# Kernel optimization log

Hardware: AMD Instinct MI355X
Metric: run time of the kernel (lower is better)

Reference implementation:

```python
import jax, jax.numpy as jnp
import numpy as np

N_NODES = 50000
N_EDGES = 800000
IN_CH = 64
HID = 128
OUT_AGE, OUT_SEX, OUT_ETH = 21, 2, 5


def _glorot(key, shape):
    fan_in, fan_out = shape
    lim = float(np.sqrt(6.0 / (fan_in + fan_out)))
    return jax.random.uniform(key, shape, jnp.float32, -lim, lim)


def sage_conv(x, src, dst, Wl, Wr, b, n_nodes):
    # PyG SAGEConv (mean aggr): out = lin_l(mean_{j->i} x_j) + lin_r(x_i) + bias
    msg_sum = jax.ops.segment_sum(x[src], dst, num_segments=n_nodes)  # [N, d]
    deg = jax.ops.segment_sum(jnp.ones((src.shape[0],), x.dtype), dst,
                              num_segments=n_nodes)  # [N]
    mean = msg_sum / jnp.maximum(deg, 1.0)[:, None]
    return mean @ Wl + x @ Wr + b


def setup_inputs() -> dict:
    key = jax.random.key(0)
    ks = jax.random.split(key, 16)
    x = jax.random.normal(ks[0], (N_NODES, IN_CH), jnp.float32)
    edge_src = jax.random.randint(ks[1], (N_EDGES,), 0, N_NODES)
    edge_dst = jax.random.randint(ks[2], (N_EDGES,), 0, N_NODES)
    dims = [(IN_CH, HID), (HID, HID), (HID, HID),
            (HID, OUT_AGE), (HID, OUT_SEX), (HID, OUT_ETH)]
    names = ['1', '2', '3', 'age', 'sex', 'eth']
    inp = {'x': x, 'edge_src': edge_src, 'edge_dst': edge_dst}
    for i, (nm, (di, do)) in enumerate(zip(names, dims)):
        inp[f'Wl_{nm}'] = _glorot(ks[3 + 2 * i], (di, do))
        inp[f'Wr_{nm}'] = _glorot(ks[4 + 2 * i], (di, do))
        inp[f'b_{nm}'] = jnp.zeros((do,), jnp.float32)
    return inp


def reference(x, edge_src, edge_dst,
              Wl_1, Wr_1, b_1, Wl_2, Wr_2, b_2, Wl_3, Wr_3, b_3,
              Wl_age, Wr_age, b_age, Wl_sex, Wr_sex, b_sex,
              Wl_eth, Wr_eth, b_eth):
    n = x.shape[0]
    h = jax.nn.relu(sage_conv(x, edge_src, edge_dst, Wl_1, Wr_1, b_1, n))
    h = jax.nn.relu(sage_conv(h, edge_src, edge_dst, Wl_2, Wr_2, b_2, n))
    h = jax.nn.relu(sage_conv(h, edge_src, edge_dst, Wl_3, Wr_3, b_3, n))
    age = sage_conv(h, edge_src, edge_dst, Wl_age, Wr_age, b_age, n)
    sex = sage_conv(h, edge_src, edge_dst, Wl_sex, Wr_sex, b_sex, n)
    eth = sage_conv(h, edge_src, edge_dst, Wl_eth, Wr_eth, b_eth, n)
    return (age, sex, eth)
```

## Files before the change

kernel.cpp:

```cpp
#include <hip/hip_runtime.h>
#include <hip/hip_bf16.h>


typedef __attribute__((ext_vector_type(8))) short bf16x8;
typedef __attribute__((ext_vector_type(4))) float f32x4;

#define NBSH 7
#define EPW  4096

__device__ __forceinline__ unsigned short f2b(float f) {
    __hip_bfloat16 h = __float2bfloat16(f);
    return *reinterpret_cast<unsigned short*>(&h);
}
__device__ __forceinline__ float b2f(unsigned short u) {
    __hip_bfloat16 h;
    *reinterpret_cast<unsigned short*>(&h) = u;
    return __bfloat162float(h);
}

__global__ void bucket_hist(const int* __restrict__ dst, int* __restrict__ ghist,
                            int n_edges, int nb) {
    __shared__ int lh[512];
    int tid = threadIdx.x;
    for (int i = tid; i < 512; i += 256) lh[i] = 0;
    __syncthreads();
    int stride = gridDim.x * blockDim.x;
    for (int e = blockIdx.x * blockDim.x + tid; e < n_edges; e += stride)
        atomicAdd(&lh[dst[e] >> NBSH], 1);
    __syncthreads();
    for (int i = tid; i < nb; i += 256)
        if (lh[i]) atomicAdd(&ghist[i], lh[i]);
}

__global__ void scan_buckets(const int* __restrict__ hist, int* __restrict__ base,
                             int* __restrict__ cur, int nb, int n_edges) {
    __shared__ int tmp[512];
    int t = threadIdx.x;
    int v = (t < nb) ? hist[t] : 0;
    tmp[t] = v;
    __syncthreads();
    for (int off = 1; off < 512; off <<= 1) {
        int u = (t >= off) ? tmp[t - off] : 0;
        __syncthreads();
        tmp[t] += u;
        __syncthreads();
    }
    if (t < nb) {
        base[t] = tmp[t] - v;
        cur[t] = tmp[t] - v;
    }
    if (t == 0) base[nb] = n_edges;
}

__global__ __launch_bounds__(512) void bin_edges_lds(
    const int* __restrict__ src, const int* __restrict__ dst,
    int* __restrict__ bkt_cur, uint2* __restrict__ ebuf, int n_edges, int nb) {
    __shared__ int hist[512];
    __shared__ int hbase[513];
    __shared__ int hcur[512];
    __shared__ uint2 sorted[EPW];
    int tid = threadIdx.x;
    int chunk0 = blockIdx.x * EPW;
    int cnt = min(EPW, n_edges - chunk0);
    hist[tid] = 0;
    __syncthreads();
    for (int i = tid; i < cnt; i += 512) atomicAdd(&hist[dst[chunk0 + i] >> NBSH], 1);
    __syncthreads();
    int v = hist[tid];
    hbase[tid] = v;
    __syncthreads();
    for (int off = 1; off < 512; off <<= 1) {
        int u = (tid >= off) ? hbase[tid - off] : 0;
        __syncthreads();
        hbase[tid] += u;
        __syncthreads();
    }
    int excl = hbase[tid] - v;
    __syncthreads();
    hbase[tid] = excl;
    hcur[tid] = excl;
    if (tid == 511) hbase[512] = excl + v;
    __syncthreads();
    for (int i = tid; i < cnt; i += 512) {
        int s = src[chunk0 + i];
        int d = dst[chunk0 + i];
        int p = atomicAdd(&hcur[d >> NBSH], 1);
        sorted[p] = make_uint2((unsigned)s, (unsigned)d);
    }
    __syncthreads();
    int cntb = hbase[tid + 1] - hbase[tid];
    int gb = 0;
    if (tid < nb && cntb > 0) gb = atomicAdd(&bkt_cur[tid], cntb);
    hist[tid] = gb;
    __syncthreads();
    for (int i = tid; i < cnt; i += 512) {
        uint2 ed = sorted[i];
        int b = (int)(ed.y >> NBSH);
        ebuf[hist[b] + (i - hbase[b])] = ed;
    }
}

__global__ void sort_bucket(const uint2* __restrict__ ebuf, const int* __restrict__ bkt_base,
                            int* __restrict__ row_start, int* __restrict__ col,
                            int n_nodes, int n_edges) {
    __shared__ int hist[128];
    __shared__ int sc[128];
    __shared__ int hcur[128];
    int b = blockIdx.x, tid = threadIdx.x;
    int lo = b << NBSH;
    if (tid < 128) hist[tid] = 0;
    __syncthreads();
    int s = bkt_base[b], t = bkt_base[b + 1];
    for (int i = s + tid; i < t; i += 256) atomicAdd(&hist[(int)ebuf[i].y - lo], 1);
    __syncthreads();
    if (tid < 128) sc[tid] = hist[tid];
    __syncthreads();
    for (int off = 1; off < 128; off <<= 1) {
        int u = (tid < 128 && tid >= off) ? sc[tid - off] : 0;
        __syncthreads();
        if (tid < 128) sc[tid] += u;
        __syncthreads();
    }
    if (tid < 128) {
        int excl = sc[tid] - hist[tid];
        hcur[tid] = excl;
        int node = lo + tid;
        if (node < n_nodes) row_start[node] = s + excl;
    }
    if (b == 0 && tid == 0) row_start[n_nodes] = n_edges;
    __syncthreads();
    for (int i = s + tid; i < t; i += 256) {
        uint2 ed = ebuf[i];
        int p = atomicAdd(&hcur[(int)ed.y - lo], 1);
        col[s + p] = (int)ed.x;
    }
}

__device__ __forceinline__ void bt_body(const float* __restrict__ Wl,
                                        const float* __restrict__ Wr,
                                        unsigned short* __restrict__ Bt,
                                        int KA, int idx) {
    int KTOT = 2 * KA;
    if (idx >= 128 * KTOT) return;
    int n = idx / KTOT, k = idx % KTOT;
    float v = (k < KA) ? Wl[k * 128 + n] : Wr[(k - KA) * 128 + n];
    Bt[idx] = f2b(v);
}

__global__ void prep_all(const float* __restrict__ x, unsigned short* __restrict__ xb, int n4,
                         const float* __restrict__ Wl1, const float* __restrict__ Wr1,
                         unsigned short* __restrict__ Bt1,
                         const float* __restrict__ Wl2, const float* __restrict__ Wr2,
                         unsigned short* __restrict__ Bt2,
                         const float* __restrict__ Wl3, const float* __restrict__ Wr3,
                         unsigned short* __restrict__ Bt3,
                         const float* __restrict__ Wl_age, const float* __restrict__ Wl_sex,
                         const float* __restrict__ Wl_eth,
                         const float* __restrict__ Wr_age, const float* __restrict__ Wr_sex,
                         const float* __restrict__ Wr_eth,
                         const float* __restrict__ b_age, const float* __restrict__ b_sex,
                         const float* __restrict__ b_eth,
                         float* __restrict__ Wl_cat, float* __restrict__ Wr_cat,
                         float* __restrict__ b_cat, int* __restrict__ bkt_hist) {
    int nbx = (n4 + 255) / 256;
    int b = blockIdx.x;
    if (b < nbx) {
        int t = b * 256 + threadIdx.x;
        if (t < n4) {
            float4 v = reinterpret_cast<const float4*>(x)[t];
            uint2 o;
            o.x = (unsigned)f2b(v.x) | ((unsigned)f2b(v.y) << 16);
            o.y = (unsigned)f2b(v.z) | ((unsigned)f2b(v.w) << 16);
            reinterpret_cast<uint2*>(xb)[t] = o;
        }
        return;
    }
    b -= nbx;
    if (b < 64)  { bt_body(Wl1, Wr1, Bt1, 64,  b * 256 + threadIdx.x); return; }
    b -= 64;
    if (b < 128) { bt_body(Wl2, Wr2, Bt2, 128, b * 256 + threadIdx.x); return; }
    b -= 128;
    if (b < 128) { bt_body(Wl3, Wr3, Bt3, 128, b * 256 + threadIdx.x); return; }
    b -= 128;
    if (b < 14) {
        int idx = b * 256 + threadIdx.x;
        if (idx < 128 * 28) {
            int k = idx / 28, j = idx % 28;
            float vl, vr;
            if (j < 21) {
                vl = Wl_age[k * 21 + j];
                vr = Wr_age[k * 21 + j];
            } else if (j < 23) {
                vl = Wl_sex[k * 2 + (j - 21)];
                vr = Wr_sex[k * 2 + (j - 21)];
            } else {
                vl = Wl_eth[k * 5 + (j - 23)];
                vr = Wr_eth[k * 5 + (j - 23)];
            }
            Wl_cat[idx] = vl;
            Wr_cat[idx] = vr;
        }
        if (idx < 28)
            b_cat[idx] = (idx < 21) ? b_age[idx] : (idx < 23) ? b_sex[idx - 21] : b_eth[idx - 23];
        return;
    }
    bkt_hist[threadIdx.x] = 0;
    bkt_hist[256 + threadIdx.x] = 0;
}

__global__ void agg128_bf(const unsigned short* __restrict__ feat,
                          const int* __restrict__ row_start, const int* __restrict__ col,
                          unsigned short* __restrict__ mean, int n_nodes) {
    int wave = (blockIdx.x * blockDim.x + threadIdx.x) >> 6;
    int lane = threadIdx.x & 63;
    if (wave >= n_nodes) return;
    int s0 = row_start[wave];
    int deg = row_start[wave + 1] - s0;
    const unsigned* f2 = reinterpret_cast<const unsigned*>(feat);
    float a0 = 0.f, a1 = 0.f, b0 = 0.f, b1 = 0.f;
    float c0 = 0.f, c1 = 0.f, d0 = 0.f, d1 = 0.f;
    for (int base = 0; base < deg; base += 64) {
        int blk = min(64, deg - base);
        int cv = col[s0 + base + min(lane, blk - 1)];
        int i = 0;
        for (; i + 3 < blk; i += 4) {
            int e0 = __shfl(cv, i), e1 = __shfl(cv, i + 1);
            int e2 = __shfl(cv, i + 2), e3 = __shfl(cv, i + 3);
            unsigned u0 = f2[(size_t)e0 * 64 + lane];
            unsigned u1 = f2[(size_t)e1 * 64 + lane];
            unsigned u2 = f2[(size_t)e2 * 64 + lane];
            unsigned u3 = f2[(size_t)e3 * 64 + lane];
            a0 += b2f((unsigned short)(u0 & 0xffff)); a1 += b2f((unsigned short)(u0 >> 16));
            b0 += b2f((unsigned short)(u1 & 0xffff)); b1 += b2f((unsigned short)(u1 >> 16));
            c0 += b2f((unsigned short)(u2 & 0xffff)); c1 += b2f((unsigned short)(u2 >> 16));
            d0 += b2f((unsigned short)(u3 & 0xffff)); d1 += b2f((unsigned short)(u3 >> 16));
        }
        for (; i < blk; ++i) {
            int e0 = __shfl(cv, i);
            unsigned u0 = f2[(size_t)e0 * 64 + lane];
            a0 += b2f((unsigned short)(u0 & 0xffff)); a1 += b2f((unsigned short)(u0 >> 16));
        }
    }
    float inv = (deg > 0) ? 1.0f / (float)deg : 0.0f;
    float sA = (a0 + b0) + (c0 + d0);
    float sB = (a1 + b1) + (c1 + d1);
    unsigned o = (unsigned)f2b(sA * inv) | ((unsigned)f2b(sB * inv) << 16);
    reinterpret_cast<unsigned*>(mean)[(size_t)wave * 64 + lane] = o;
}

__global__ void agg64_bf(const unsigned short* __restrict__ feat,
                         const int* __restrict__ row_start, const int* __restrict__ col,
                         unsigned short* __restrict__ mean, int n_nodes) {
    int wave = (blockIdx.x * blockDim.x + threadIdx.x) >> 6;
    int lane = threadIdx.x & 63;
    if (wave >= n_nodes) return;
    int half = lane >> 5;
    int lp = lane & 31;
    int s0 = row_start[wave];
    int deg = row_start[wave + 1] - s0;
    const unsigned* f2 = reinterpret_cast<const unsigned*>(feat);
    float a0 = 0.f, a1 = 0.f, b0 = 0.f, b1 = 0.f;
    float c0 = 0.f, c1 = 0.f, d0 = 0.f, d1 = 0.f;
    for (int base = 0; base < deg; base += 64) {
        int blk = min(64, deg - base);
        int cv = col[s0 + base + min(lane, blk - 1)];
        int nfull = blk & ~7;
        for (int i = half * 4; i < nfull; i += 8) {
            int e0 = __shfl(cv, i), e1 = __shfl(cv, i + 1);
            int e2 = __shfl(cv, i + 2), e3 = __shfl(cv, i + 3);
            unsigned u0 = f2[(size_t)e0 * 32 + lp];
            unsigned u1 = f2[(size_t)e1 * 32 + lp];
            unsigned u2 = f2[(size_t)e2 * 32 + lp];
            unsigned u3 = f2[(size_t)e3 * 32 + lp];
            a0 += b2f((unsigned short)(u0 & 0xffff)); a1 += b2f((unsigned short)(u0 >> 16));
            b0 += b2f((unsigned short)(u1 & 0xffff)); b1 += b2f((unsigned short)(u1 >> 16));
            c0 += b2f((unsigned short)(u2 & 0xffff)); c1 += b2f((unsigned short)(u2 >> 16));
            d0 += b2f((unsigned short)(u3 & 0xffff)); d1 += b2f((unsigned short)(u3 >> 16));
        }
        int tstart = nfull + half * 4;
        int tend = min(blk, tstart + 4);
        for (int i = tstart; i < tend; ++i) {
            int e0 = __shfl(cv, i);
            unsigned u0 = f2[(size_t)e0 * 32 + lp];
            a0 += b2f((unsigned short)(u0 & 0xffff)); a1 += b2f((unsigned short)(u0 >> 16));
        }
    }
    float sA = (a0 + b0) + (c0 + d0);
    float sB = (a1 + b1) + (c1 + d1);
    sA += __shfl_down(sA, 32);
    sB += __shfl_down(sB, 32);
    if (half == 0) {
        float inv = (deg > 0) ? 1.0f / (float)deg : 0.0f;
        unsigned o = (unsigned)f2b(sA * inv) | ((unsigned)f2b(sB * inv) << 16);
        reinterpret_cast<unsigned*>(mean)[(size_t)wave * 32 + lp] = o;
    }
}

template <int KTOT, int KA>
__global__ __launch_bounds__(256) void mfma_layer(
    const unsigned short* __restrict__ A0, const unsigned short* __restrict__ A1,
    const unsigned short* __restrict__ Bt, const float* __restrict__ bias,
    unsigned short* __restrict__ out, int n_nodes) {
    constexpr int KC = KTOT / 64;
    __shared__ __align__(16) unsigned short sA[64][72];
    __shared__ __align__(16) unsigned short sB[128][72];
    int node0 = blockIdx.x * 64;
    int tid = threadIdx.x;
    int w = tid >> 6, lane = tid & 63;
    f32x4 acc[8] = {};
    for (int kc = 0; kc < KC; ++kc) {
        const unsigned short* Asrc;
        int kbase, aw;
        if (kc * 64 < KA) { Asrc = A0; kbase = kc * 64; aw = KA; }
        else              { Asrc = A1; kbase = kc * 64 - KA; aw = KTOT - KA; }
        {
            int nd = tid >> 2, k16 = (tid & 3) * 16;
            uint4 v0 = {0, 0, 0, 0}, v1 = {0, 0, 0, 0};
            int gn = node0 + nd;
            if (gn < n_nodes) {
                const uint4* src = reinterpret_cast<const uint4*>(Asrc + (size_t)gn * aw + kbase + k16);
                v0 = src[0];
                v1 = src[1];
            }
            uint4* dst = reinterpret_cast<uint4*>(&sA[nd][k16]);
            dst[0] = v0;
            dst[1] = v1;
        }
        {
            int n = tid >> 1, k32 = (tid & 1) * 32;
            const uint4* src = reinterpret_cast<const uint4*>(Bt + (size_t)n * KTOT + kc * 64 + k32);
            uint4* dst = reinterpret_cast<uint4*>(&sB[n][k32]);
            dst[0] = src[0];
            dst[1] = src[1];
            dst[2] = src[2];
            dst[3] = src[3];
        }
        __syncthreads();
#pragma unroll
        for (int ks = 0; ks < 2; ++ks) {
            int kl = ks * 32 + (lane >> 4) * 8;
            bf16x8 af = *reinterpret_cast<const bf16x8*>(&sA[w * 16 + (lane & 15)][kl]);
#pragma unroll
            for (int t = 0; t < 8; ++t) {
                bf16x8 bfr = *reinterpret_cast<const bf16x8*>(&sB[t * 16 + (lane & 15)][kl]);
                acc[t] = __builtin_amdgcn_mfma_f32_16x16x32_bf16(af, bfr, acc[t], 0, 0, 0);
            }
        }
        __syncthreads();
    }
    int r0 = w * 16, cq = lane >> 4, cr = lane & 15;
#pragma unroll
    for (int t = 0; t < 8; ++t) {
        int colj = t * 16 + cr;
        float bv = bias[colj];
#pragma unroll
        for (int i = 0; i < 4; ++i) {
            int node = node0 + r0 + cq * 4 + i;
            if (node < n_nodes) {
                float v = fmaxf(acc[t][i] + bv, 0.0f);
                out[(size_t)node * 128 + colj] = f2b(v);
            }
        }
    }
}

__global__ void proj2_kernel(const unsigned short* __restrict__ h,
                             const float* __restrict__ Wl_cat, const float* __restrict__ Wr_cat,
                             const float* __restrict__ b_cat,
                             float* __restrict__ p, float* __restrict__ q, int n_nodes) {
    const int NPB = 4;
    int node0 = blockIdx.x * NPB;
    __shared__ float sh[NPB][128];
    for (int idx = threadIdx.x; idx < NPB * 128; idx += blockDim.x) {
        int n = idx >> 7, k = idx & 127;
        int node = node0 + n;
        if (node < n_nodes) sh[n][k] = b2f(h[(size_t)node * 128 + k]);
    }
    __syncthreads();
    int n = threadIdx.x >> 5, j = threadIdx.x & 31;
    int node = node0 + n;
    if (node >= n_nodes) return;
    float accp = 0.f;
    float accq = 0.f;
    if (j < 28) {
        accq = b_cat[j];
        for (int k = 0; k < 128; k++) {
            float hv = sh[n][k];
            accp += hv * Wl_cat[k * 28 + j];
            accq += hv * Wr_cat[k * 28 + j];
        }
    }
    p[(size_t)node * 32 + j] = accp;
    q[(size_t)node * 32 + j] = accq;
}

__global__ void head_final(const float* __restrict__ p, const float* __restrict__ q,
                           const int* __restrict__ row_start, const int* __restrict__ col,
                           float* __restrict__ age, float* __restrict__ sex,
                           float* __restrict__ eth, int n_nodes) {
    int node = (blockIdx.x * blockDim.x + threadIdx.x) >> 5;
    int lane = threadIdx.x & 63;
    int lp = lane & 31;
    int grpbase = lane & 32;
    if (node >= n_nodes) return;
    int s0 = row_start[node];
    int deg = row_start[node + 1] - s0;
    float a = 0.f, b = 0.f, c = 0.f, d = 0.f;
    for (int base = 0; base < deg; base += 32) {
        int blk = min(32, deg - base);
        int cv = col[s0 + base + min(lp, blk - 1)];
        int i = 0;
        for (; i + 3 < blk; i += 4) {
            int e0 = __shfl(cv, grpbase + i),     e1 = __shfl(cv, grpbase + i + 1);
            int e2 = __shfl(cv, grpbase + i + 2), e3 = __shfl(cv, grpbase + i + 3);
            a += p[(size_t)e0 * 32 + lp];
            b += p[(size_t)e1 * 32 + lp];
            c += p[(size_t)e2 * 32 + lp];
            d += p[(size_t)e3 * 32 + lp];
        }
        for (; i < blk; ++i) {
            int e0 = __shfl(cv, grpbase + i);
            a += p[(size_t)e0 * 32 + lp];
        }
    }
    float inv = (deg > 0) ? 1.0f / (float)deg : 0.0f;
    float out = ((a + b) + (c + d)) * inv + q[(size_t)node * 32 + lp];
    if (lp < 21)
        age[(size_t)node * 21 + lp] = out;
    else if (lp < 23)
        sex[(size_t)node * 2 + (lp - 21)] = out;
    else if (lp < 28)
        eth[(size_t)node * 5 + (lp - 23)] = out;
}

extern "C" void kernel_launch(void* const* d_in, const int* in_sizes, int n_in,
                              void* d_out, int out_size, void* d_ws, size_t ws_size,
                              hipStream_t stream) {
    const float* x        = (const float*)d_in[0];
    const int*   edge_src = (const int*)d_in[1];
    const int*   edge_dst = (const int*)d_in[2];
    const float* Wl_1 = (const float*)d_in[3];
    const float* Wr_1 = (const float*)d_in[4];
    const float* b_1  = (const float*)d_in[5];
    const float* Wl_2 = (const float*)d_in[6];
    const float* Wr_2 = (const float*)d_in[7];
    const float* b_2  = (const float*)d_in[8];
    const float* Wl_3 = (const float*)d_in[9];
    const float* Wr_3 = (const float*)d_in[10];
    const float* b_3  = (const float*)d_in[11];
    const float* Wl_age = (const float*)d_in[12];
    const float* Wr_age = (const float*)d_in[13];
    const float* b_age  = (const float*)d_in[14];
    const float* Wl_sex = (const float*)d_in[15];
    const float* Wr_sex = (const float*)d_in[16];
    const float* b_sex  = (const float*)d_in[17];
    const float* Wl_eth = (const float*)d_in[18];
    const float* Wr_eth = (const float*)d_in[19];
    const float* b_eth  = (const float*)d_in[20];

    const int n_nodes = in_sizes[0] / 64;
    const int n_edges = in_sizes[1];

    char* ws = (char*)d_ws;
    int*            row_start = (int*)(ws + 200192);
    int*            col       = (int*)(ws + 600576);
    unsigned short* Bt1       = (unsigned short*)(ws + 3800832);
    unsigned short* Bt2       = (unsigned short*)(ws + 3833600);
    unsigned short* Bt3       = (unsigned short*)(ws + 3899136);
    float*          Wl_cat    = (float*)(ws + 3964672);
    float*          Wr_cat    = (float*)(ws + 3979008);
    float*          b_cat     = (float*)(ws + 3993344);
    unsigned short* xb        = (unsigned short*)(ws + 3993600);
    unsigned short* h_bf      = (unsigned short*)(ws + 10393856);
    unsigned short* mean_bf   = (unsigned short*)(ws + 23194112);
    float*          p         = (float*)(ws + 35994368);
    float*          q         = (float*)(ws + 42394624);
    uint2*          ebuf      = (uint2*)p;
    int*            bkt_hist  = (int*)q;
    int*            bkt_base  = bkt_hist + 512;
    int*            bkt_cur   = bkt_hist + 1032;

    float* out_age = (float*)d_out;
    float* out_sex = out_age + (size_t)n_nodes * 21;
    float* out_eth = out_sex + (size_t)n_nodes * 2;

    const int nb      = (n_nodes + 127) >> NBSH;
    const int nchunks = (n_edges + EPW - 1) / EPW;
    const int n4      = n_nodes * 64 / 4;

    {
        int grid = (n4 + 255) / 256 + 64 + 128 + 128 + 14 + 1;
        prep_all<<<grid, 256, 0, stream>>>(
            x, xb, n4, Wl_1, Wr_1, Bt1, Wl_2, Wr_2, Bt2, Wl_3, Wr_3, Bt3,
            Wl_age, Wl_sex, Wl_eth, Wr_age, Wr_sex, Wr_eth, b_age, b_sex, b_eth,
            Wl_cat, Wr_cat, b_cat, bkt_hist);
    }

    bucket_hist<<<256, 256, 0, stream>>>(edge_dst, bkt_hist, n_edges, nb);
    scan_buckets<<<1, 512, 0, stream>>>(bkt_hist, bkt_base, bkt_cur, nb, n_edges);
    bin_edges_lds<<<nchunks, 512, 0, stream>>>(edge_src, edge_dst, bkt_cur, ebuf, n_edges, nb);
    sort_bucket<<<nb, 256, 0, stream>>>(ebuf, bkt_base, row_start, col, n_nodes, n_edges);

    const int agg_grid  = (n_nodes * 64 + 255) / 256;
    const int gemm_grid = (n_nodes + 63) / 64;

    agg64_bf<<<agg_grid, 256, 0, stream>>>(xb, row_start, col, mean_bf, n_nodes);
    mfma_layer<128, 64><<<gemm_grid, 256, 0, stream>>>(mean_bf, xb, Bt1, b_1, h_bf, n_nodes);

    agg128_bf<<<agg_grid, 256, 0, stream>>>(h_bf, row_start, col, mean_bf, n_nodes);
    mfma_layer<256, 128><<<gemm_grid, 256, 0, stream>>>(mean_bf, h_bf, Bt2, b_2, h_bf, n_nodes);

    agg128_bf<<<agg_grid, 256, 0, stream>>>(h_bf, row_start, col, mean_bf, n_nodes);
    mfma_layer<256, 128><<<gemm_grid, 256, 0, stream>>>(mean_bf, h_bf, Bt3, b_3, h_bf, n_nodes);

    proj2_kernel<<<(n_nodes + 3) / 4, 128, 0, stream>>>(h_bf, Wl_cat, Wr_cat, b_cat, p, q, n_nodes);
    head_final<<<(n_nodes * 32 + 255) / 256, 256, 0, stream>>>(
        p, q, row_start, col, out_age, out_sex, out_eth, n_nodes);
}
```

Baseline: 330.4 us.

## Tile head projection over 64 nodes per block with weights staged in LDS

The head projection kernel now handles 64 nodes per 256-thread block instead of 4 nodes per 128-thread block. Both weight matrices are staged in shared memory, and each thread accumulates 8 nodes so every weight load is reused across them. Node features are loaded with 16-byte vector reads. This cuts repeated global weight reads and launch granularity, at the cost of about 60KB of LDS per block, which may limit occupancy.

Measured after the change: 316.4 us. 1.04x faster.

```diff
diff --git a/kernel.cpp b/kernel.cpp
--- a/kernel.cpp
+++ b/kernel.cpp
@@ -364,34 +364,62 @@
     }
 }
 
-__global__ void proj2_kernel(const unsigned short* __restrict__ h,
-                             const float* __restrict__ Wl_cat, const float* __restrict__ Wr_cat,
-                             const float* __restrict__ b_cat,
-                             float* __restrict__ p, float* __restrict__ q, int n_nodes) {
-    const int NPB = 4;
-    int node0 = blockIdx.x * NPB;
-    __shared__ float sh[NPB][128];
-    for (int idx = threadIdx.x; idx < NPB * 128; idx += blockDim.x) {
-        int n = idx >> 7, k = idx & 127;
+__global__ __launch_bounds__(256) void proj2_kernel(
+    const unsigned short* __restrict__ h,
+    const float* __restrict__ Wl_cat, const float* __restrict__ Wr_cat,
+    const float* __restrict__ b_cat,
+    float* __restrict__ p, float* __restrict__ q, int n_nodes) {
+    __shared__ float sh[64][128];
+    __shared__ float swl[128 * 28];
+    __shared__ float swr[128 * 28];
+    int node0 = blockIdx.x * 64;
+    int tid = threadIdx.x;
+    for (int i = tid; i < 128 * 28; i += 256) {
+        swl[i] = Wl_cat[i];
+        swr[i] = Wr_cat[i];
+    }
+    for (int it = tid; it < 1024; it += 256) {
+        int n = it >> 4, k8 = (it & 15) * 8;
         int node = node0 + n;
-        if (node < n_nodes) sh[n][k] = b2f(h[(size_t)node * 128 + k]);
-    }
-    __syncthreads();
-    int n = threadIdx.x >> 5, j = threadIdx.x & 31;
-    int node = node0 + n;
-    if (node >= n_nodes) return;
-    float accp = 0.f;
-    float accq = 0.f;
+        if (node < n_nodes) {
+            uint4 u = *reinterpret_cast<const uint4*>(h + (size_t)node * 128 + k8);
+            sh[n][k8 + 0] = b2f((unsigned short)(u.x & 0xffff));
+            sh[n][k8 + 1] = b2f((unsigned short)(u.x >> 16));
+            sh[n][k8 + 2] = b2f((unsigned short)(u.y & 0xffff));
+            sh[n][k8 + 3] = b2f((unsigned short)(u.y >> 16));
+            sh[n][k8 + 4] = b2f((unsigned short)(u.z & 0xffff));
+            sh[n][k8 + 5] = b2f((unsigned short)(u.z >> 16));
+            sh[n][k8 + 6] = b2f((unsigned short)(u.w & 0xffff));
+            sh[n][k8 + 7] = b2f((unsigned short)(u.w >> 16));
+        } else {
+            for (int z = 0; z < 8; ++z) sh[n][k8 + z] = 0.f;
+        }
+    }
+    __syncthreads();
+    int j = tid & 31, ng = tid >> 5;
+    float accp[8] = {};
+    float accq[8] = {};
     if (j < 28) {
-        accq = b_cat[j];
-        for (int k = 0; k < 128; k++) {
-            float hv = sh[n][k];
-            accp += hv * Wl_cat[k * 28 + j];
-            accq += hv * Wr_cat[k * 28 + j];
-        }
-    }
-    p[(size_t)node * 32 + j] = accp;
-    q[(size_t)node * 32 + j] = accq;
+        for (int k = 0; k < 128; k += 2) {
+            float wl0 = swl[k * 28 + j],       wr0 = swr[k * 28 + j];
+            float wl1 = swl[(k + 1) * 28 + j], wr1 = swr[(k + 1) * 28 + j];
+#pragma unroll
+            for (int i = 0; i < 8; ++i) {
+                float2 hv = *reinterpret_cast<const float2*>(&sh[ng * 8 + i][k]);
+                accp[i] += hv.x * wl0 + hv.y * wl1;
+                accq[i] += hv.x * wr0 + hv.y * wr1;
+            }
+        }
+    }
+    float bj = (j < 28) ? b_cat[j] : 0.f;
+#pragma unroll
+    for (int i = 0; i < 8; ++i) {
+        int node = node0 + ng * 8 + i;
+        if (node < n_nodes) {
+            p[(size_t)node * 32 + j] = (j < 28) ? accp[i] : 0.f;
+            q[(size_t)node * 32 + j] = (j < 28) ? (accq[i] + bj) : 0.f;
+        }
+    }
 }
 
 __global__ void head_final(const float* __restrict__ p, const float* __restrict__ q,
@@ -513,7 +541,7 @@
     agg128_bf<<<agg_grid, 256, 0, stream>>>(h_bf, row_start, col, mean_bf, n_nodes);
     mfma_layer<256, 128><<<gemm_grid, 256, 0, stream>>>(mean_bf, h_bf, Bt3, b_3, h_bf, n_nodes);
 
-    proj2_kernel<<<(n_nodes + 3) / 4, 128, 0, stream>>>(h_bf, Wl_cat, Wr_cat, b_cat, p, q, n_nodes);
+    proj2_kernel<<<(n_nodes + 63) / 64, 256, 0, stream>>>(h_bf, Wl_cat, Wr_cat, b_cat, p, q, n_nodes);
     head_final<<<(n_nodes * 32 + 255) / 256, 256, 0, stream>>>(
         p, q, row_start, col, out_age, out_sex, out_eth, n_nodes);
 }
```
